# Kernel optimization log

Measured on AMD Instinct MI355X. Metric: run time of the kernel, lower is better.

Reference implementation:

```python
import jax, jax.numpy as jnp
import numpy as np

H = 64   # hidden size
V = 29   # vocab / feature size
SOS = 27 # start-token index set to 1 in the initial one-hot


def _cell(x, h, c, Wih, Whh, bih, bhh):
    # PyTorch LSTMCell gate order: i, f, g, o
    g = x @ Wih.T + h @ Whh.T + bih + bhh
    i, f, gg, o = jnp.split(g, 4, axis=-1)
    c = jax.nn.sigmoid(f) * c + jax.nn.sigmoid(i) * jnp.tanh(gg)
    h = jax.nn.sigmoid(o) * jnp.tanh(c)
    return h, c


def setup_inputs() -> dict:
    key = jax.random.key(0)
    ks = iter(jax.random.split(key, 32))
    T, B = 1024, 512
    def p(shape, scale=0.05):
        return jax.random.normal(next(ks), shape, dtype=jnp.float32) * scale
    inp = {"input_seq": jax.random.normal(next(ks), (T, B, V), dtype=jnp.float32)}
    inp.update(
        enc_Wih0=p((4 * H, V)), enc_Whh0=p((4 * H, H)), enc_bih0=p((4 * H,)), enc_bhh0=p((4 * H,)),
        enc_Wih1=p((4 * H, H)), enc_Whh1=p((4 * H, H)), enc_bih1=p((4 * H,)), enc_bhh1=p((4 * H,)),
        d1_Wih=p((4 * H, V)), d1_Whh=p((4 * H, H)), d1_bih=p((4 * H,)), d1_bhh=p((4 * H,)),
        d2_Wih=p((4 * H, H)), d2_Whh=p((4 * H, H)), d2_bih=p((4 * H,)), d2_bhh=p((4 * H,)),
        cls_W=p((V, H)), cls_b=p((V,)),
    )
    return inp


def reference(input_seq, enc_Wih0, enc_Whh0, enc_bih0, enc_bhh0,
              enc_Wih1, enc_Whh1, enc_bih1, enc_bhh1,
              d1_Wih, d1_Whh, d1_bih, d1_bhh,
              d2_Wih, d2_Whh, d2_bih, d2_bhh,
              cls_W, cls_b):
    T, B, _ = input_seq.shape
    dt = input_seq.dtype
    z = jnp.zeros((B, H), dt)

    def layer(x_seq, Wih, Whh, bih, bhh):
        def step(carry, x):
            h, c = _cell(x, carry[0], carry[1], Wih, Whh, bih, bhh)
            return (h, c), h
        (h, c), ys = jax.lax.scan(step, (z, z), x_seq)
        return ys, h, c

    # 2-layer encoder LSTM with zero initial state
    y1, _, _ = layer(input_seq, enc_Wih0, enc_Whh0, enc_bih0, enc_bhh0)
    _, h1, c1 = layer(y1, enc_Wih1, enc_Whh1, enc_bih1, enc_bhh1)  # top-layer final (h, c)

    let0 = jnp.zeros((B, V), dt).at[:, SOS].set(1.0)

    def dec_step(carry, _):
        h1, c1, h2, c2, let = carry
        h1, c1 = _cell(let, h1, c1, d1_Wih, d1_Whh, d1_bih, d1_bhh)
        h2, c2 = _cell(h1, h2, c2, d2_Wih, d2_Whh, d2_bih, d2_bhh)
        pred = h2 @ cls_W.T + cls_b  # [B, V]
        idx = jnp.argmax(pred, axis=-1)  # [B]
        # Faithful to original bug: sets column idx[b] to 1 for ALL rows, for each b
        let = jnp.zeros((B, V), pred.dtype).at[:, idx].set(1.0)
        return (h1, c1, h2, c2, let), pred

    _, outputs = jax.lax.scan(dec_step, (h1, c1, z, z, let0), None, length=T)
    return outputs  # [T, B, V]
```

## Files before the change

kernel.cpp:

```cpp
#include <hip/hip_runtime.h>
#include <math.h>

#define TSTEPS 1024
#define BATCH  512
#define HID    64
#define VOC    29
#define SOS    27
#define MASK29 0x1FFFFFFFu

#define ENC_BLOCKS 256
#define DEC_BLOCKS 256
#define NTHREADS   512

__device__ __forceinline__ float frcp(float x){ return __builtin_amdgcn_rcpf(x); }
__device__ __forceinline__ float sigmf(float x){ return frcp(1.0f + __expf(-x)); }
__device__ __forceinline__ float tanhfast(float x){ return 1.0f - 2.0f*frcp(1.0f + __expf(2.0f*x)); }

__global__ __attribute__((amdgpu_flat_work_group_size(NTHREADS,NTHREADS), amdgpu_waves_per_eu(2,2)))
void enc_kernel(const float* __restrict__ x,
                const float* __restrict__ Wih0, const float* __restrict__ Whh0,
                const float* __restrict__ bih0, const float* __restrict__ bhh0,
                const float* __restrict__ Wih1, const float* __restrict__ Whh1,
                const float* __restrict__ bih1, const float* __restrict__ bhh1,
                float* __restrict__ h1g, float* __restrict__ c1g)
{
  const int tid = threadIdx.x;
  const int b0  = blockIdx.x * 2;
  const bool g0 = tid < 256;
  const int  r  = g0 ? tid : (tid-256);

  __shared__ __align__(16) float xs[2][32];
  __shared__ __align__(16) float h0s[2][HID], h1s[2][HID];
  __shared__ __align__(16) float gA[2][256], gB[2][256];

  float wh[64], w2[64];
  if (g0){
    #pragma unroll
    for (int k=0;k<64;k++) wh[k] = Whh0[r*64+k];
    #pragma unroll
    for (int k=0;k<29;k++) w2[k] = Wih0[r*29+k];
    #pragma unroll
    for (int k=29;k<64;k++) w2[k] = 0.f;
  } else {
    #pragma unroll
    for (int k=0;k<64;k++){ wh[k] = Whh1[r*64+k]; w2[k] = Wih1[r*64+k]; }
  }
  const float bias = g0 ? (bih0[r]+bhh0[r]) : (bih1[r]+bhh1[r]);

  float creg = 0.f;
  if (tid < 128){ int u=tid>>6,k=tid&63; h0s[u][k]=0.f; h1s[u][k]=0.f; }

  const int pidx = tid - 448;
  const bool pf  = (pidx >= 0) && (pidx < 2*VOC);
  const int prow = pf ? (pidx/VOC) : 0;
  const int pcol = pf ? (pidx%VOC) : 0;
  if (pf) xs[prow][pcol] = x[(size_t)(b0+prow)*VOC + pcol];
  __syncthreads();

  for (int t=0;t<=TSTEPS;t++){
    float xv = 0.f;
    if (pf && t+1 < TSTEPS)
      xv = x[(size_t)(t+1)*BATCH*VOC + (size_t)(b0+prow)*VOC + pcol];

    if (g0){
      if (t < TSTEPS){
        #pragma unroll
        for (int u=0;u<2;u++){
          float a0=bias,a1=0.f,a2=0.f,a3=0.f;
          const float4* xv4 = (const float4*)xs[u];
          #pragma unroll
          for (int c=0;c<7;c++){
            float4 q=xv4[c];
            a0=fmaf(q.x,w2[4*c+0],a0); a1=fmaf(q.y,w2[4*c+1],a1);
            a2=fmaf(q.z,w2[4*c+2],a2); a3=fmaf(q.w,w2[4*c+3],a3);
          }
          a0=fmaf(xs[u][28],w2[28],a0);
          const float4* h4=(const float4*)h0s[u];
          #pragma unroll
          for (int c=0;c<16;c++){
            float4 q=h4[c];
            a0=fmaf(q.x,wh[4*c+0],a0); a1=fmaf(q.y,wh[4*c+1],a1);
            a2=fmaf(q.z,wh[4*c+2],a2); a3=fmaf(q.w,wh[4*c+3],a3);
          }
          gA[u][r]=(a0+a1)+(a2+a3);
        }
      }
    } else {
      if (t >= 1){
        #pragma unroll
        for (int u=0;u<2;u++){
          float a0=bias,a1=0.f,a2=0.f,a3=0.f;
          const float4* i4=(const float4*)h0s[u];
          const float4* h4=(const float4*)h1s[u];
          #pragma unroll
          for (int c=0;c<16;c++){
            float4 q=i4[c], w=h4[c];
            a0=fmaf(q.x,w2[4*c+0],a0); a1=fmaf(q.y,w2[4*c+1],a1);
            a2=fmaf(q.z,w2[4*c+2],a2); a3=fmaf(q.w,w2[4*c+3],a3);
            a0=fmaf(w.x,wh[4*c+0],a0); a1=fmaf(w.y,wh[4*c+1],a1);
            a2=fmaf(w.z,wh[4*c+2],a2); a3=fmaf(w.w,wh[4*c+3],a3);
          }
          gB[u][r]=(a0+a1)+(a2+a3);
        }
      }
    }
    __syncthreads();
    if (tid < 128){
      if (t < TSTEPS){
        int u=tid>>6,k=tid&63;
        float ig=gA[u][k],fg=gA[u][64+k],gg=gA[u][128+k],og=gA[u][192+k];
        float c=sigmf(fg)*creg + sigmf(ig)*tanhfast(gg);
        creg=c; h0s[u][k]=sigmf(og)*tanhfast(c);
      }
    } else if (tid < 384){
      if (t >= 1){
        int tt=tid-256,u=tt>>6,k=tt&63;
        float ig=gB[u][k],fg=gB[u][64+k],gg=gB[u][128+k],og=gB[u][192+k];
        float c=sigmf(fg)*creg + sigmf(ig)*tanhfast(gg);
        creg=c; h1s[u][k]=sigmf(og)*tanhfast(c);
      }
    }
    if (pf && t+1 < TSTEPS) xs[prow][pcol] = xv;
    __syncthreads();
  }

  if (tid >= 256 && tid < 384){
    int tt=tid-256,u=tt>>6,k=tt&63;
    h1g[(b0+u)*HID+k]=h1s[u][k];
    c1g[(b0+u)*HID+k]=creg;
  }
}

__global__ __attribute__((amdgpu_flat_work_group_size(NTHREADS,NTHREADS), amdgpu_waves_per_eu(2,2)))
void dec_kernel(const float* __restrict__ h1gp, const float* __restrict__ c1gp,
                const float* __restrict__ W1ih, const float* __restrict__ W1hh,
                const float* __restrict__ b1ih, const float* __restrict__ b1hh,
                const float* __restrict__ W2ih, const float* __restrict__ W2hh,
                const float* __restrict__ b2ih, const float* __restrict__ b2hh,
                const float* __restrict__ clsW, const float* __restrict__ clsb,
                float* __restrict__ out,
                unsigned long long* __restrict__ lvl1)
{
  const int tid  = threadIdx.x;
  const int r    = tid >> 1;
  const int p    = tid & 1;
  const int b0   = blockIdx.x * 2;
  const unsigned grp = blockIdx.x & 15;
  const unsigned idx = blockIdx.x >> 4;

  __shared__ __align__(16) float clsW_s[VOC][68];
  __shared__ __align__(16) float clsb_s[32];
  __shared__ __align__(16) float gl[2][256];
  __shared__ __align__(16) float h1s[2][HID], h2s[2][HID];
  __shared__ unsigned maskLDS;

  for (int i=tid;i<VOC*HID;i+=NTHREADS) clsW_s[i/HID][i%HID] = clsW[i];
  if (tid<VOC) clsb_s[tid]=clsb[tid];

  float w1h[32], w2i[32], w2h[32], wi1c[15];
  #pragma unroll
  for (int k=0;k<32;k++){
    w1h[k]=W1hh[r*HID+32*p+k];
    w2i[k]=W2ih[r*HID+32*p+k];
    w2h[k]=W2hh[r*HID+32*p+k];
  }
  const int cbase = p ? 15 : 0;
  const int cn    = p ? 14 : 15;
  #pragma unroll
  for (int j=0;j<15;j++) wi1c[j] = (j<cn) ? W1ih[r*VOC+cbase+j] : 0.f;
  const float biasg = p ? 0.f : (b1ih[r]+b1hh[r]);
  const float bias2 = p ? 0.f : (b2ih[r]+b2hh[r]);

  float c1reg=0.f, c2reg=0.f;
  if (tid<128){
    int u=tid>>6,k=tid&63;
    h1s[u][k]=h1gp[(b0+u)*HID+k];
    c1reg    =c1gp[(b0+u)*HID+k];
    h2s[u][k]=0.f;
  }
  __syncthreads();

  float hd1[2];
  #pragma unroll
  for (int u=0;u<2;u++){
    float a0=0.f,a1=0.f,a2=0.f,a3=0.f;
    const float4* h4=(const float4*)(h1s[u]+32*p);
    #pragma unroll
    for (int c=0;c<8;c++){
      float4 q=h4[c];
      a0=fmaf(q.x,w1h[4*c+0],a0); a1=fmaf(q.y,w1h[4*c+1],a1);
      a2=fmaf(q.z,w1h[4*c+2],a2); a3=fmaf(q.w,w1h[4*c+3],a3);
    }
    hd1[u]=(a0+a1)+(a2+a3);
  }

  unsigned mask = 1u<<SOS;

  for (int s=0;s<TSTEPS;s++){
    #pragma unroll
    for (int u=0;u<2;u++){
      float it = biasg;
      #pragma unroll
      for (int j=0;j<15;j++)
        it += ((mask>>(cbase+j))&1u) ? wi1c[j] : 0.f;
      float v = it + hd1[u];
      v += __shfl_xor(v,1);
      if (!p) gl[u][r] = v;
    }
    __syncthreads();
    if (tid<128){
      int u=tid>>6,k=tid&63;
      float ig=gl[u][k],fg=gl[u][64+k],gg=gl[u][128+k],og=gl[u][192+k];
      float c=sigmf(fg)*c1reg+sigmf(ig)*tanhfast(gg);
      c1reg=c; h1s[u][k]=sigmf(og)*tanhfast(c);
    }
    __syncthreads();
    #pragma unroll
    for (int u=0;u<2;u++){
      float a0=bias2,a1=0.f,a2=0.f,a3=0.f;
      const float4* i4=(const float4*)(h1s[u]+32*p);
      const float4* h4=(const float4*)(h2s[u]+32*p);
      #pragma unroll
      for (int c=0;c<8;c++){
        float4 q=i4[c], w=h4[c];
        a0=fmaf(q.x,w2i[4*c+0],a0); a1=fmaf(q.y,w2i[4*c+1],a1);
        a2=fmaf(q.z,w2i[4*c+2],a2); a3=fmaf(q.w,w2i[4*c+3],a3);
        a0=fmaf(w.x,w2h[4*c+0],a0); a1=fmaf(w.y,w2h[4*c+1],a1);
        a2=fmaf(w.z,w2h[4*c+2],a2); a3=fmaf(w.w,w2h[4*c+3],a3);
      }
      float v=(a0+a1)+(a2+a3);
      v += __shfl_xor(v,1);
      if (!p) gl[u][r]=v;
    }
    __syncthreads();
    if (tid<128){
      int u=tid>>6,k=tid&63;
      float ig=gl[u][k],fg=gl[u][64+k],gg=gl[u][128+k],og=gl[u][192+k];
      float c=sigmf(fg)*c2reg+sigmf(ig)*tanhfast(gg);
      c2reg=c; h2s[u][k]=sigmf(og)*tanhfast(c);
    }
    __syncthreads();
    if (tid<64){
      int row=tid>>5, v=tid&31;
      float pv = -INFINITY;
      if (v<VOC){
        float a0=clsb_s[v],a1=0.f,a2=0.f,a3=0.f;
        const float4* h4=(const float4*)h2s[row];
        #pragma unroll
        for (int c=0;c<16;c++){
          float4 q=h4[c];
          a0=fmaf(q.x,clsW_s[v][4*c+0],a0); a1=fmaf(q.y,clsW_s[v][4*c+1],a1);
          a2=fmaf(q.z,clsW_s[v][4*c+2],a2); a3=fmaf(q.w,clsW_s[v][4*c+3],a3);
        }
        pv=(a0+a1)+(a2+a3);
        out[((size_t)s*BATCH + (size_t)(b0+row))*VOC + v]=pv;
      }
      int ix=v;
      #pragma unroll
      for (int off=16; off>0; off>>=1){
        float ov=__shfl_xor(pv,off);
        int   oi=__shfl_xor(ix,off);
        if (ov>pv || (ov==pv && oi<ix)){ pv=ov; ix=oi; }
      }
      unsigned bit = 1u<<ix;
      unsigned mb  = bit | __shfl_xor(bit,32);
      if (tid==0 && s+1<TSTEPS)
        __hip_atomic_fetch_or(&lvl1[(size_t)grp*TSTEPS+s],
                              (unsigned long long)mb | (1ULL<<(32+idx)),
                              __ATOMIC_RELAXED, __HIP_MEMORY_SCOPE_AGENT);
    }
    if (s+1<TSTEPS){
      #pragma unroll
      for (int u=0;u<2;u++){
        float a0=0.f,a1=0.f,a2=0.f,a3=0.f;
        const float4* h4=(const float4*)(h1s[u]+32*p);
        #pragma unroll
        for (int c=0;c<8;c++){
          float4 q=h4[c];
          a0=fmaf(q.x,w1h[4*c+0],a0); a1=fmaf(q.y,w1h[4*c+1],a1);
          a2=fmaf(q.z,w1h[4*c+2],a2); a3=fmaf(q.w,w1h[4*c+3],a3);
        }
        hd1[u]=(a0+a1)+(a2+a3);
      }
      if (tid<64){
        while (true){
          unsigned long long u64 = 0;
          if (tid<16)
            u64 = __hip_atomic_load(&lvl1[(size_t)tid*TSTEPS+s],
                                    __ATOMIC_RELAXED, __HIP_MEMORY_SCOPE_AGENT);
          bool ok = (tid>=16) || ((unsigned)(u64>>32) == 0xFFFFu);
          if (__ballot(ok) == ~0ull){
            unsigned m = (tid<16) ? ((unsigned)u64 & MASK29) : 0u;
            m |= __shfl_xor(m,1); m |= __shfl_xor(m,2);
            m |= __shfl_xor(m,4); m |= __shfl_xor(m,8);
            if (tid==0) maskLDS = m;
            break;
          }
        }
      }
      __syncthreads();
      mask = maskLDS;
    }
  }
}

extern "C" void kernel_launch(void* const* d_in, const int* in_sizes, int n_in,
                              void* d_out, int out_size, void* d_ws, size_t ws_size,
                              hipStream_t stream)
{
  const float* x     = (const float*)d_in[0];
  const float* eWih0 = (const float*)d_in[1];
  const float* eWhh0 = (const float*)d_in[2];
  const float* ebih0 = (const float*)d_in[3];
  const float* ebhh0 = (const float*)d_in[4];
  const float* eWih1 = (const float*)d_in[5];
  const float* eWhh1 = (const float*)d_in[6];
  const float* ebih1 = (const float*)d_in[7];
  const float* ebhh1 = (const float*)d_in[8];
  const float* d1Wih = (const float*)d_in[9];
  const float* d1Whh = (const float*)d_in[10];
  const float* d1bih = (const float*)d_in[11];
  const float* d1bhh = (const float*)d_in[12];
  const float* d2Wih = (const float*)d_in[13];
  const float* d2Whh = (const float*)d_in[14];
  const float* d2bih = (const float*)d_in[15];
  const float* d2bhh = (const float*)d_in[16];
  const float* clsW  = (const float*)d_in[17];
  const float* clsb  = (const float*)d_in[18];
  float* out = (float*)d_out;

  float* h1g = (float*)d_ws;
  float* c1g = h1g + BATCH*HID;
  unsigned long long* lvl1 = (unsigned long long*)((char*)d_ws + (size_t)(2*BATCH*HID)*sizeof(float));

  hipMemsetAsync(lvl1, 0, 16*TSTEPS*sizeof(unsigned long long), stream);

  enc_kernel<<<ENC_BLOCKS, NTHREADS, 0, stream>>>(
      x, eWih0,eWhh0,ebih0,ebhh0, eWih1,eWhh1,ebih1,ebhh1, h1g,c1g);

  void* args[] = { (void*)&h1g, (void*)&c1g,
                   (void*)&d1Wih,(void*)&d1Whh,(void*)&d1bih,(void*)&d1bhh,
                   (void*)&d2Wih,(void*)&d2Whh,(void*)&d2bih,(void*)&d2bhh,
                   (void*)&clsW,(void*)&clsb,(void*)&out,(void*)&lvl1 };
  hipLaunchCooperativeKernel((void*)dec_kernel, dim3(DEC_BLOCKS), dim3(NTHREADS),
                             args, 0, stream);
}
```

Measured before the change: 5.822 ms.

## Speculate constant decoder mask over adaptive windows with verification and rollback

Replaces the per-step grid-wide mask exchange with speculative execution. Each block runs a window of decoder steps assuming the one-hot feedback mask stays unchanged, publishing each step's argmax bits. A single flag barrier at the end of the window then checks whether any step's combined mask differed. The window doubles, up to 16 steps, while speculation holds. On a mismatch the kernel restores checkpointed state and replays only the valid prefix. This trades one global sync per step for one per window, at the cost of wasted work and replay when the mask changes often.

```diff
diff --git a/kernel.cpp b/kernel.cpp
--- a/kernel.cpp
+++ b/kernel.cpp
@@ -6,11 +6,11 @@
 #define HID    64
 #define VOC    29
 #define SOS    27
-#define MASK29 0x1FFFFFFFu
 
 #define ENC_BLOCKS 256
 #define DEC_BLOCKS 256
 #define NTHREADS   512
+#define WMAX       16
 
 __device__ __forceinline__ float frcp(float x){ return __builtin_amdgcn_rcpf(x); }
 __device__ __forceinline__ float sigmf(float x){ return frcp(1.0f + __expf(-x)); }
@@ -139,20 +139,20 @@
                 const float* __restrict__ b2ih, const float* __restrict__ b2hh,
                 const float* __restrict__ clsW, const float* __restrict__ clsb,
                 float* __restrict__ out,
-                unsigned long long* __restrict__ lvl1)
+                unsigned* __restrict__ flags, unsigned* __restrict__ masks)
 {
   const int tid  = threadIdx.x;
   const int r    = tid >> 1;
   const int p    = tid & 1;
   const int b0   = blockIdx.x * 2;
-  const unsigned grp = blockIdx.x & 15;
-  const unsigned idx = blockIdx.x >> 4;
+  const int blk  = blockIdx.x;
 
   __shared__ __align__(16) float clsW_s[VOC][68];
   __shared__ __align__(16) float clsb_s[32];
   __shared__ __align__(16) float gl[2][256];
   __shared__ __align__(16) float h1s[2][HID], h2s[2][HID];
-  __shared__ unsigned maskLDS;
+  __shared__ __align__(16) float h1ck[2][HID], h2ck[2][HID];
+  __shared__ unsigned u_lds[WMAX];
 
   for (int i=tid;i<VOC*HID;i+=NTHREADS) clsW_s[i/HID][i%HID] = clsW[i];
   if (tid<VOC) clsb_s[tid]=clsb[tid];
@@ -194,82 +194,94 @@
     hd1[u]=(a0+a1)+(a2+a3);
   }
 
-  unsigned mask = 1u<<SOS;
-
-  for (int s=0;s<TSTEPS;s++){
-    #pragma unroll
-    for (int u=0;u<2;u++){
-      float it = biasg;
+  unsigned F = 1u<<SOS;
+  int f = 0;
+  unsigned rr = 0;
+  int Wcur = 4;
+
+  while (f < TSTEPS){
+    const int Wr = (TSTEPS - f < Wcur) ? (TSTEPS - f) : Wcur;
+
+    const float c1ck=c1reg, c2ck=c2reg, hd10=hd1[0], hd11=hd1[1];
+    if (tid<128){ int u=tid>>6,k=tid&63; h1ck[u][k]=h1s[u][k]; h2ck[u][k]=h2s[u][k]; }
+
+    float it0 = biasg;
+    #pragma unroll
+    for (int jj=0;jj<15;jj++) it0 += ((F>>(cbase+jj))&1u) ? wi1c[jj] : 0.f;
+
+    unsigned* __restrict__ mrow = masks + (rr&1u)*(WMAX*256);
+
+    for (int j=0;j<Wr;j++){
       #pragma unroll
-      for (int j=0;j<15;j++)
-        it += ((mask>>(cbase+j))&1u) ? wi1c[j] : 0.f;
-      float v = it + hd1[u];
-      v += __shfl_xor(v,1);
-      if (!p) gl[u][r] = v;
-    }
-    __syncthreads();
-    if (tid<128){
-      int u=tid>>6,k=tid&63;
-      float ig=gl[u][k],fg=gl[u][64+k],gg=gl[u][128+k],og=gl[u][192+k];
-      float c=sigmf(fg)*c1reg+sigmf(ig)*tanhfast(gg);
-      c1reg=c; h1s[u][k]=sigmf(og)*tanhfast(c);
-    }
-    __syncthreads();
-    #pragma unroll
-    for (int u=0;u<2;u++){
-      float a0=bias2,a1=0.f,a2=0.f,a3=0.f;
-      const float4* i4=(const float4*)(h1s[u]+32*p);
-      const float4* h4=(const float4*)(h2s[u]+32*p);
+      for (int u=0;u<2;u++){
+        float v = it0 + hd1[u];
+        v += __shfl_xor(v,1);
+        if (!p) gl[u][r] = v;
+      }
+      __syncthreads();
+      if (tid<128){
+        int u=tid>>6,k=tid&63;
+        float ig=gl[u][k],fg=gl[u][64+k],gg=gl[u][128+k],og=gl[u][192+k];
+        float c=sigmf(fg)*c1reg+sigmf(ig)*tanhfast(gg);
+        c1reg=c; h1s[u][k]=sigmf(og)*tanhfast(c);
+      }
+      __syncthreads();
       #pragma unroll
-      for (int c=0;c<8;c++){
-        float4 q=i4[c], w=h4[c];
-        a0=fmaf(q.x,w2i[4*c+0],a0); a1=fmaf(q.y,w2i[4*c+1],a1);
-        a2=fmaf(q.z,w2i[4*c+2],a2); a3=fmaf(q.w,w2i[4*c+3],a3);
-        a0=fmaf(w.x,w2h[4*c+0],a0); a1=fmaf(w.y,w2h[4*c+1],a1);
-        a2=fmaf(w.z,w2h[4*c+2],a2); a3=fmaf(w.w,w2h[4*c+3],a3);
-      }
-      float v=(a0+a1)+(a2+a3);
-      v += __shfl_xor(v,1);
-      if (!p) gl[u][r]=v;
-    }
-    __syncthreads();
-    if (tid<128){
-      int u=tid>>6,k=tid&63;
-      float ig=gl[u][k],fg=gl[u][64+k],gg=gl[u][128+k],og=gl[u][192+k];
-      float c=sigmf(fg)*c2reg+sigmf(ig)*tanhfast(gg);
-      c2reg=c; h2s[u][k]=sigmf(og)*tanhfast(c);
-    }
-    __syncthreads();
-    if (tid<64){
-      int row=tid>>5, v=tid&31;
-      float pv = -INFINITY;
-      if (v<VOC){
-        float a0=clsb_s[v],a1=0.f,a2=0.f,a3=0.f;
-        const float4* h4=(const float4*)h2s[row];
-        #pragma unroll
-        for (int c=0;c<16;c++){
-          float4 q=h4[c];
-          a0=fmaf(q.x,clsW_s[v][4*c+0],a0); a1=fmaf(q.y,clsW_s[v][4*c+1],a1);
-          a2=fmaf(q.z,clsW_s[v][4*c+2],a2); a3=fmaf(q.w,clsW_s[v][4*c+3],a3);
-        }
-        pv=(a0+a1)+(a2+a3);
-        out[((size_t)s*BATCH + (size_t)(b0+row))*VOC + v]=pv;
-      }
-      int ix=v;
-      #pragma unroll
-      for (int off=16; off>0; off>>=1){
-        float ov=__shfl_xor(pv,off);
-        int   oi=__shfl_xor(ix,off);
-        if (ov>pv || (ov==pv && oi<ix)){ pv=ov; ix=oi; }
-      }
-      unsigned bit = 1u<<ix;
-      unsigned mb  = bit | __shfl_xor(bit,32);
-      if (tid==0 && s+1<TSTEPS)
-        __hip_atomic_fetch_or(&lvl1[(size_t)grp*TSTEPS+s],
-                              (unsigned long long)mb | (1ULL<<(32+idx)),
-                              __ATOMIC_RELAXED, __HIP_MEMORY_SCOPE_AGENT);
-    }
-    if (s+1<TSTEPS){
+      for (int u=0;u<2;u++){
+        float a0=bias2,a1=0.f,a2=0.f,a3=0.f;
+        const float4* i4=(const float4*)(h1s[u]+32*p);
+        const float4* h4=(const float4*)(h2s[u]+32*p);
+        #pragma unroll
+        for (int c=0;c<8;c++){
+          float4 q=i4[c], w=h4[c];
+          a0=fmaf(q.x,w2i[4*c+0],a0); a1=fmaf(q.y,w2i[4*c+1],a1);
+          a2=fmaf(q.z,w2i[4*c+2],a2); a3=fmaf(q.w,w2i[4*c+3],a3);
+          a0=fmaf(w.x,w2h[4*c+0],a0); a1=fmaf(w.y,w2h[4*c+1],a1);
+          a2=fmaf(w.z,w2h[4*c+2],a2); a3=fmaf(w.w,w2h[4*c+3],a3);
+        }
+        float v=(a0+a1)+(a2+a3);
+        v += __shfl_xor(v,1);
+        if (!p) gl[u][r]=v;
+      }
+      __syncthreads();
+      if (tid<128){
+        int u=tid>>6,k=tid&63;
+        float ig=gl[u][k],fg=gl[u][64+k],gg=gl[u][128+k],og=gl[u][192+k];
+        float c=sigmf(fg)*c2reg+sigmf(ig)*tanhfast(gg);
+        c2reg=c; h2s[u][k]=sigmf(og)*tanhfast(c);
+      }
+      __syncthreads();
+      if (tid<64){
+        const int s = f + j;
+        int row=tid>>5, v=tid&31;
+        float pv = -INFINITY;
+        if (v<VOC){
+          float a0=clsb_s[v],a1=0.f,a2=0.f,a3=0.f;
+          const float4* h4=(const float4*)h2s[row];
+          #pragma unroll
+          for (int c=0;c<16;c++){
+            float4 q=h4[c];
+            a0=fmaf(q.x,clsW_s[v][4*c+0],a0); a1=fmaf(q.y,clsW_s[v][4*c+1],a1);
+            a2=fmaf(q.z,clsW_s[v][4*c+2],a2); a3=fmaf(q.w,clsW_s[v][4*c+3],a3);
+          }
+          pv=(a0+a1)+(a2+a3);
+          out[((size_t)s*BATCH + (size_t)(b0+row))*VOC + v]=pv;
+        }
+        int ix=v;
+        #pragma unroll
+        for (int off=16; off>0; off>>=1){
+          float ov=__shfl_xor(pv,off);
+          int   oi=__shfl_xor(ix,off);
+          if (ov>pv || (ov==pv && oi<ix)){ pv=ov; ix=oi; }
+        }
+        unsigned bit = 1u<<ix;
+        unsigned mb  = bit | __shfl_xor(bit,32);
+        if (tid==0){
+          __hip_atomic_store(&mrow[j*256+blk], mb, __ATOMIC_RELAXED, __HIP_MEMORY_SCOPE_AGENT);
+          if (j==Wr-1)
+            __hip_atomic_store(&flags[blk], rr+1u, __ATOMIC_RELEASE, __HIP_MEMORY_SCOPE_AGENT);
+        }
+      }
       #pragma unroll
       for (int u=0;u<2;u++){
         float a0=0.f,a1=0.f,a2=0.f,a3=0.f;
@@ -282,24 +294,103 @@
         }
         hd1[u]=(a0+a1)+(a2+a3);
       }
-      if (tid<64){
-        while (true){
-          unsigned long long u64 = 0;
-          if (tid<16)
-            u64 = __hip_atomic_load(&lvl1[(size_t)tid*TSTEPS+s],
-                                    __ATOMIC_RELAXED, __HIP_MEMORY_SCOPE_AGENT);
-          bool ok = (tid>=16) || ((unsigned)(u64>>32) == 0xFFFFu);
-          if (__ballot(ok) == ~0ull){
-            unsigned m = (tid<16) ? ((unsigned)u64 & MASK29) : 0u;
-            m |= __shfl_xor(m,1); m |= __shfl_xor(m,2);
-            m |= __shfl_xor(m,4); m |= __shfl_xor(m,8);
-            if (tid==0) maskLDS = m;
-            break;
-          }
-        }
-      }
-      __syncthreads();
-      mask = maskLDS;
+    }
+
+    if (tid<64){
+      const unsigned tgt = rr+1u;
+      for(;;){
+        unsigned a=__hip_atomic_load(&flags[tid    ],__ATOMIC_RELAXED,__HIP_MEMORY_SCOPE_AGENT);
+        unsigned b=__hip_atomic_load(&flags[tid+ 64],__ATOMIC_RELAXED,__HIP_MEMORY_SCOPE_AGENT);
+        unsigned c=__hip_atomic_load(&flags[tid+128],__ATOMIC_RELAXED,__HIP_MEMORY_SCOPE_AGENT);
+        unsigned d=__hip_atomic_load(&flags[tid+192],__ATOMIC_RELAXED,__HIP_MEMORY_SCOPE_AGENT);
+        bool ok = (a>=tgt)&&(b>=tgt)&&(c>=tgt)&&(d>=tgt);
+        if (__ballot(ok)==~0ull) break;
+      }
+      __threadfence();
+    }
+    __syncthreads();
+
+    {
+      const int j = tid>>5, sub = tid&31;
+      if (j < Wr){
+        unsigned* mp = mrow + j*256;
+        unsigned um=0;
+        #pragma unroll
+        for (int q=0;q<8;q++)
+          um |= __hip_atomic_load(&mp[q*32+sub],__ATOMIC_RELAXED,__HIP_MEMORY_SCOPE_AGENT);
+        um |= __shfl_xor(um,1); um |= __shfl_xor(um,2);
+        um |= __shfl_xor(um,4); um |= __shfl_xor(um,8); um |= __shfl_xor(um,16);
+        if (sub==0) u_lds[j]=um;
+      }
+    }
+    __syncthreads();
+
+    int jstar = Wr;
+    for (int jj=1;jj<Wr;jj++){ if (u_lds[jj-1]!=F){ jstar=jj; break; } }
+
+    if (jstar==Wr){
+      F = u_lds[Wr-1];
+      f += Wr; rr++;
+      Wcur = (2*Wcur>WMAX)?WMAX:2*Wcur;
+    } else {
+      c1reg=c1ck; c2reg=c2ck; hd1[0]=hd10; hd1[1]=hd11;
+      if (tid<128){ int u=tid>>6,k=tid&63; h1s[u][k]=h1ck[u][k]; h2s[u][k]=h2ck[u][k]; }
+      for (int j2=0;j2<jstar;j2++){
+        #pragma unroll
+        for (int u=0;u<2;u++){
+          float v = it0 + hd1[u];
+          v += __shfl_xor(v,1);
+          if (!p) gl[u][r] = v;
+        }
+        __syncthreads();
+        if (tid<128){
+          int u=tid>>6,k=tid&63;
+          float ig=gl[u][k],fg=gl[u][64+k],gg=gl[u][128+k],og=gl[u][192+k];
+          float c=sigmf(fg)*c1reg+sigmf(ig)*tanhfast(gg);
+          c1reg=c; h1s[u][k]=sigmf(og)*tanhfast(c);
+        }
+        __syncthreads();
+        #pragma unroll
+        for (int u=0;u<2;u++){
+          float a0=bias2,a1=0.f,a2=0.f,a3=0.f;
+          const float4* i4=(const float4*)(h1s[u]+32*p);
+          const float4* h4=(const float4*)(h2s[u]+32*p);
+          #pragma unroll
+          for (int c=0;c<8;c++){
+            float4 q=i4[c], w=h4[c];
+            a0=fmaf(q.x,w2i[4*c+0],a0); a1=fmaf(q.y,w2i[4*c+1],a1);
+            a2=fmaf(q.z,w2i[4*c+2],a2); a3=fmaf(q.w,w2i[4*c+3],a3);
+            a0=fmaf(w.x,w2h[4*c+0],a0); a1=fmaf(w.y,w2h[4*c+1],a1);
+            a2=fmaf(w.z,w2h[4*c+2],a2); a3=fmaf(w.w,w2h[4*c+3],a3);
+          }
+          float v=(a0+a1)+(a2+a3);
+          v += __shfl_xor(v,1);
+          if (!p) gl[u][r]=v;
+        }
+        __syncthreads();
+        if (tid<128){
+          int u=tid>>6,k=tid&63;
+          float ig=gl[u][k],fg=gl[u][64+k],gg=gl[u][128+k],og=gl[u][192+k];
+          float c=sigmf(fg)*c2reg+sigmf(ig)*tanhfast(gg);
+          c2reg=c; h2s[u][k]=sigmf(og)*tanhfast(c);
+        }
+        __syncthreads();
+        #pragma unroll
+        for (int u=0;u<2;u++){
+          float a0=0.f,a1=0.f,a2=0.f,a3=0.f;
+          const float4* h4=(const float4*)(h1s[u]+32*p);
+          #pragma unroll
+          for (int c=0;c<8;c++){
+            float4 q=h4[c];
+            a0=fmaf(q.x,w1h[4*c+0],a0); a1=fmaf(q.y,w1h[4*c+1],a1);
+            a2=fmaf(q.z,w1h[4*c+2],a2); a3=fmaf(q.w,w1h[4*c+3],a3);
+          }
+          hd1[u]=(a0+a1)+(a2+a3);
+        }
+      }
+      F = u_lds[jstar-1];
+      f += jstar; rr++;
+      Wcur = jstar;
     }
   }
 }
@@ -331,9 +422,10 @@
 
   float* h1g = (float*)d_ws;
   float* c1g = h1g + BATCH*HID;
-  unsigned long long* lvl1 = (unsigned long long*)((char*)d_ws + (size_t)(2*BATCH*HID)*sizeof(float));
-
-  hipMemsetAsync(lvl1, 0, 16*TSTEPS*sizeof(unsigned long long), stream);
+  unsigned* flags = (unsigned*)(c1g + BATCH*HID);
+  unsigned* masks = flags + 256;
+
+  hipMemsetAsync(flags, 0, 256*sizeof(unsigned), stream);
 
   enc_kernel<<<ENC_BLOCKS, NTHREADS, 0, stream>>>(
       x, eWih0,eWhh0,ebih0,ebhh0, eWih1,eWhh1,ebih1,ebhh1, h1g,c1g);
@@ -341,7 +433,8 @@
   void* args[] = { (void*)&h1g, (void*)&c1g,
                    (void*)&d1Wih,(void*)&d1Whh,(void*)&d1bih,(void*)&d1bhh,
                    (void*)&d2Wih,(void*)&d2Whh,(void*)&d2bih,(void*)&d2bhh,
-                   (void*)&clsW,(void*)&clsb,(void*)&out,(void*)&lvl1 };
+                   (void*)&clsW,(void*)&clsb,(void*)&out,
+                   (void*)&flags,(void*)&masks };
   hipLaunchCooperativeKernel((void*)dec_kernel, dim3(DEC_BLOCKS), dim3(NTHREADS),
                              args, 0, stream);
 }
```

Measured after the change: 4.847 ms. 16.8% less time.

## Speculate decoder steps with a constant letter mask and roll back on mismatch

Applied to the files above, without the earlier changes.

The decoder now runs a window of steps assuming the global argmax mask stays unchanged, writes each step's per-block mask with a round tag, and only does a grid-wide check after the window. If any step's global mask differs from the assumed one, state is restored from per-step checkpoints in shared memory and execution resumes from the first wrong step. The window size grows adaptively. Gate rows are also regrouped so each 8-lane group holds all four gates, which removes the shared-memory gate exchange and one barrier per cell. This trades the per-step grid synchronization for wasted recomputation whenever the argmax mask changes, and adds checkpoint stores and LDS usage.

```diff
diff --git a/kernel.cpp b/kernel.cpp
--- a/kernel.cpp
+++ b/kernel.cpp
@@ -11,6 +11,7 @@
 #define ENC_BLOCKS 256
 #define DEC_BLOCKS 256
 #define NTHREADS   512
+#define WMAX       16
 
 __device__ __forceinline__ float frcp(float x){ return __builtin_amdgcn_rcpf(x); }
 __device__ __forceinline__ float sigmf(float x){ return frcp(1.0f + __expf(-x)); }
@@ -139,20 +140,23 @@
                 const float* __restrict__ b2ih, const float* __restrict__ b2hh,
                 const float* __restrict__ clsW, const float* __restrict__ clsb,
                 float* __restrict__ out,
-                unsigned long long* __restrict__ lvl1)
+                unsigned long long* __restrict__ mseq)
 {
   const int tid  = threadIdx.x;
+  const int p    = tid & 1;
   const int r    = tid >> 1;
-  const int p    = tid & 1;
-  const int b0   = blockIdx.x * 2;
-  const unsigned grp = blockIdx.x & 15;
-  const unsigned idx = blockIdx.x >> 4;
+  const int q    = r & 3;
+  const int m    = tid >> 3;
+  const int g    = q*64 + m;
+  const int blk  = blockIdx.x;
+  const int b0   = blk * 2;
 
   __shared__ __align__(16) float clsW_s[VOC][68];
   __shared__ __align__(16) float clsb_s[32];
-  __shared__ __align__(16) float gl[2][256];
-  __shared__ __align__(16) float h1s[2][HID], h2s[2][HID];
-  __shared__ unsigned maskLDS;
+  __shared__ __align__(16) float h1s[2][2][HID], h2s[2][2][HID];
+  __shared__ __align__(16) float h1ck[WMAX][2][HID], c1ck[WMAX][2][HID];
+  __shared__ __align__(16) float h2ck[WMAX][2][HID], c2ck[WMAX][2][HID];
+  __shared__ unsigned u_lds[WMAX];
 
   for (int i=tid;i<VOC*HID;i+=NTHREADS) clsW_s[i/HID][i%HID] = clsW[i];
   if (tid<VOC) clsb_s[tid]=clsb[tid];
@@ -160,147 +164,171 @@
   float w1h[32], w2i[32], w2h[32], wi1c[15];
   #pragma unroll
   for (int k=0;k<32;k++){
-    w1h[k]=W1hh[r*HID+32*p+k];
-    w2i[k]=W2ih[r*HID+32*p+k];
-    w2h[k]=W2hh[r*HID+32*p+k];
+    w1h[k]=W1hh[g*HID+32*p+k];
+    w2i[k]=W2ih[g*HID+32*p+k];
+    w2h[k]=W2hh[g*HID+32*p+k];
   }
   const int cbase = p ? 15 : 0;
   const int cn    = p ? 14 : 15;
   #pragma unroll
-  for (int j=0;j<15;j++) wi1c[j] = (j<cn) ? W1ih[r*VOC+cbase+j] : 0.f;
-  const float biasg = p ? 0.f : (b1ih[r]+b1hh[r]);
-  const float bias2 = p ? 0.f : (b2ih[r]+b2hh[r]);
-
-  float c1reg=0.f, c2reg=0.f;
+  for (int j=0;j<15;j++) wi1c[j] = (j<cn) ? W1ih[g*VOC+cbase+j] : 0.f;
+  const float biasg = p ? 0.f : (b1ih[g]+b1hh[g]);
+  const float bias2 = p ? 0.f : (b2ih[g]+b2hh[g]);
+
+  float c1r[2], c2r[2];
+  c1r[0]=c1gp[(b0+0)*HID+m]; c1r[1]=c1gp[(b0+1)*HID+m];
+  c2r[0]=0.f; c2r[1]=0.f;
   if (tid<128){
     int u=tid>>6,k=tid&63;
-    h1s[u][k]=h1gp[(b0+u)*HID+k];
-    c1reg    =c1gp[(b0+u)*HID+k];
-    h2s[u][k]=0.f;
+    h1s[0][u][k]=h1gp[(b0+u)*HID+k];
+    h2s[0][u][k]=0.f;
   }
   __syncthreads();
 
-  float hd1[2];
-  #pragma unroll
-  for (int u=0;u<2;u++){
-    float a0=0.f,a1=0.f,a2=0.f,a3=0.f;
-    const float4* h4=(const float4*)(h1s[u]+32*p);
-    #pragma unroll
-    for (int c=0;c<8;c++){
-      float4 q=h4[c];
-      a0=fmaf(q.x,w1h[4*c+0],a0); a1=fmaf(q.y,w1h[4*c+1],a1);
-      a2=fmaf(q.z,w1h[4*c+2],a2); a3=fmaf(q.w,w1h[4*c+3],a3);
-    }
-    hd1[u]=(a0+a1)+(a2+a3);
-  }
-
-  unsigned mask = 1u<<SOS;
-
-  for (int s=0;s<TSTEPS;s++){
-    #pragma unroll
-    for (int u=0;u<2;u++){
-      float it = biasg;
-      #pragma unroll
-      for (int j=0;j<15;j++)
-        it += ((mask>>(cbase+j))&1u) ? wi1c[j] : 0.f;
-      float v = it + hd1[u];
-      v += __shfl_xor(v,1);
-      if (!p) gl[u][r] = v;
-    }
-    __syncthreads();
-    if (tid<128){
-      int u=tid>>6,k=tid&63;
-      float ig=gl[u][k],fg=gl[u][64+k],gg=gl[u][128+k],og=gl[u][192+k];
-      float c=sigmf(fg)*c1reg+sigmf(ig)*tanhfast(gg);
-      c1reg=c; h1s[u][k]=sigmf(og)*tanhfast(c);
-    }
-    __syncthreads();
-    #pragma unroll
-    for (int u=0;u<2;u++){
-      float a0=bias2,a1=0.f,a2=0.f,a3=0.f;
-      const float4* i4=(const float4*)(h1s[u]+32*p);
-      const float4* h4=(const float4*)(h2s[u]+32*p);
-      #pragma unroll
-      for (int c=0;c<8;c++){
-        float4 q=i4[c], w=h4[c];
-        a0=fmaf(q.x,w2i[4*c+0],a0); a1=fmaf(q.y,w2i[4*c+1],a1);
-        a2=fmaf(q.z,w2i[4*c+2],a2); a3=fmaf(q.w,w2i[4*c+3],a3);
-        a0=fmaf(w.x,w2h[4*c+0],a0); a1=fmaf(w.y,w2h[4*c+1],a1);
-        a2=fmaf(w.z,w2h[4*c+2],a2); a3=fmaf(w.w,w2h[4*c+3],a3);
-      }
-      float v=(a0+a1)+(a2+a3);
-      v += __shfl_xor(v,1);
-      if (!p) gl[u][r]=v;
-    }
-    __syncthreads();
-    if (tid<128){
-      int u=tid>>6,k=tid&63;
-      float ig=gl[u][k],fg=gl[u][64+k],gg=gl[u][128+k],og=gl[u][192+k];
-      float c=sigmf(fg)*c2reg+sigmf(ig)*tanhfast(gg);
-      c2reg=c; h2s[u][k]=sigmf(og)*tanhfast(c);
-    }
-    __syncthreads();
-    if (tid<64){
-      int row=tid>>5, v=tid&31;
-      float pv = -INFINITY;
-      if (v<VOC){
-        float a0=clsb_s[v],a1=0.f,a2=0.f,a3=0.f;
-        const float4* h4=(const float4*)h2s[row];
-        #pragma unroll
-        for (int c=0;c<16;c++){
-          float4 q=h4[c];
-          a0=fmaf(q.x,clsW_s[v][4*c+0],a0); a1=fmaf(q.y,clsW_s[v][4*c+1],a1);
-          a2=fmaf(q.z,clsW_s[v][4*c+2],a2); a3=fmaf(q.w,clsW_s[v][4*c+3],a3);
-        }
-        pv=(a0+a1)+(a2+a3);
-        out[((size_t)s*BATCH + (size_t)(b0+row))*VOC + v]=pv;
-      }
-      int ix=v;
-      #pragma unroll
-      for (int off=16; off>0; off>>=1){
-        float ov=__shfl_xor(pv,off);
-        int   oi=__shfl_xor(ix,off);
-        if (ov>pv || (ov==pv && oi<ix)){ pv=ov; ix=oi; }
-      }
-      unsigned bit = 1u<<ix;
-      unsigned mb  = bit | __shfl_xor(bit,32);
-      if (tid==0 && s+1<TSTEPS)
-        __hip_atomic_fetch_or(&lvl1[(size_t)grp*TSTEPS+s],
-                              (unsigned long long)mb | (1ULL<<(32+idx)),
-                              __ATOMIC_RELAXED, __HIP_MEMORY_SCOPE_AGENT);
-    }
-    if (s+1<TSTEPS){
+  unsigned F = 1u<<SOS;
+  int f = 0;
+  unsigned rr = 0;
+  int Wcur = 4, streak = 0;
+  int pb = 0;
+
+  while (f < TSTEPS){
+    const int Wr = (TSTEPS - f < Wcur) ? (TSTEPS - f) : Wcur;
+    const unsigned tag = rr + 1u;
+    unsigned long long* __restrict__ mrow = mseq + (size_t)(rr&1u)*(WMAX*256);
+
+    if (tid < Wr) u_lds[tid] = 0u;
+
+    float it0 = biasg;
+    #pragma unroll
+    for (int jj=0;jj<15;jj++) it0 += ((F>>(cbase+jj))&1u) ? wi1c[jj] : 0.f;
+
+    for (int j=0;j<Wr;j++){
+      float h1n[2];
       #pragma unroll
       for (int u=0;u<2;u++){
-        float a0=0.f,a1=0.f,a2=0.f,a3=0.f;
-        const float4* h4=(const float4*)(h1s[u]+32*p);
+        float a0=it0,a1=0.f,a2=0.f,a3=0.f;
+        const float4* h4=(const float4*)(&h1s[pb][u][32*p]);
         #pragma unroll
         for (int c=0;c<8;c++){
-          float4 q=h4[c];
-          a0=fmaf(q.x,w1h[4*c+0],a0); a1=fmaf(q.y,w1h[4*c+1],a1);
-          a2=fmaf(q.z,w1h[4*c+2],a2); a3=fmaf(q.w,w1h[4*c+3],a3);
-        }
-        hd1[u]=(a0+a1)+(a2+a3);
-      }
+          float4 qv=h4[c];
+          a0=fmaf(qv.x,w1h[4*c+0],a0); a1=fmaf(qv.y,w1h[4*c+1],a1);
+          a2=fmaf(qv.z,w1h[4*c+2],a2); a3=fmaf(qv.w,w1h[4*c+3],a3);
+        }
+        float v=(a0+a1)+(a2+a3);
+        v += __shfl_xor(v,1);
+        float x2=__shfl_xor(v,2), x4=__shfl_xor(v,4), x6=__shfl_xor(v,6);
+        float ig = q==0?v : q==1?x2 : q==2?x4 : x6;
+        float fg = q==1?v : q==0?x2 : q==3?x4 : x6;
+        float gg = q==2?v : q==3?x2 : q==0?x4 : x6;
+        float og = q==3?v : q==2?x2 : q==1?x4 : x6;
+        float c = sigmf(fg)*c1r[u] + sigmf(ig)*tanhfast(gg);
+        c1r[u]=c; h1n[u]=sigmf(og)*tanhfast(c);
+      }
+      if ((tid&7)==0){
+        h1s[pb^1][0][m]=h1n[0]; h1s[pb^1][1][m]=h1n[1];
+        h1ck[j][0][m]=h1n[0];   h1ck[j][1][m]=h1n[1];
+        c1ck[j][0][m]=c1r[0];   c1ck[j][1][m]=c1r[1];
+      }
+      __syncthreads();
+
+      float h2n[2];
+      #pragma unroll
+      for (int u=0;u<2;u++){
+        float a0=bias2,a1=0.f,a2=0.f,a3=0.f;
+        const float4* i4=(const float4*)(&h1s[pb^1][u][32*p]);
+        const float4* h4=(const float4*)(&h2s[pb][u][32*p]);
+        #pragma unroll
+        for (int c=0;c<8;c++){
+          float4 qv=i4[c], wv=h4[c];
+          a0=fmaf(qv.x,w2i[4*c+0],a0); a1=fmaf(qv.y,w2i[4*c+1],a1);
+          a2=fmaf(qv.z,w2i[4*c+2],a2); a3=fmaf(qv.w,w2i[4*c+3],a3);
+          a0=fmaf(wv.x,w2h[4*c+0],a0); a1=fmaf(wv.y,w2h[4*c+1],a1);
+          a2=fmaf(wv.z,w2h[4*c+2],a2); a3=fmaf(wv.w,w2h[4*c+3],a3);
+        }
+        float v=(a0+a1)+(a2+a3);
+        v += __shfl_xor(v,1);
+        float x2=__shfl_xor(v,2), x4=__shfl_xor(v,4), x6=__shfl_xor(v,6);
+        float ig = q==0?v : q==1?x2 : q==2?x4 : x6;
+        float fg = q==1?v : q==0?x2 : q==3?x4 : x6;
+        float gg = q==2?v : q==3?x2 : q==0?x4 : x6;
+        float og = q==3?v : q==2?x2 : q==1?x4 : x6;
+        float c = sigmf(fg)*c2r[u] + sigmf(ig)*tanhfast(gg);
+        c2r[u]=c; h2n[u]=sigmf(og)*tanhfast(c);
+      }
+      if ((tid&7)==0){
+        h2s[pb^1][0][m]=h2n[0]; h2s[pb^1][1][m]=h2n[1];
+        h2ck[j][0][m]=h2n[0];   h2ck[j][1][m]=h2n[1];
+        c2ck[j][0][m]=c2r[0];   c2ck[j][1][m]=c2r[1];
+      }
+      __syncthreads();
+
       if (tid<64){
-        while (true){
-          unsigned long long u64 = 0;
-          if (tid<16)
-            u64 = __hip_atomic_load(&lvl1[(size_t)tid*TSTEPS+s],
-                                    __ATOMIC_RELAXED, __HIP_MEMORY_SCOPE_AGENT);
-          bool ok = (tid>=16) || ((unsigned)(u64>>32) == 0xFFFFu);
-          if (__ballot(ok) == ~0ull){
-            unsigned m = (tid<16) ? ((unsigned)u64 & MASK29) : 0u;
-            m |= __shfl_xor(m,1); m |= __shfl_xor(m,2);
-            m |= __shfl_xor(m,4); m |= __shfl_xor(m,8);
-            if (tid==0) maskLDS = m;
-            break;
+        const int s = f + j;
+        int row=tid>>5, v=tid&31;
+        float pv = -INFINITY;
+        if (v<VOC){
+          float a0=clsb_s[v],a1=0.f,a2=0.f,a3=0.f;
+          const float4* h4=(const float4*)h2s[pb^1][row];
+          #pragma unroll
+          for (int c=0;c<16;c++){
+            float4 qv=h4[c];
+            a0=fmaf(qv.x,clsW_s[v][4*c+0],a0); a1=fmaf(qv.y,clsW_s[v][4*c+1],a1);
+            a2=fmaf(qv.z,clsW_s[v][4*c+2],a2); a3=fmaf(qv.w,clsW_s[v][4*c+3],a3);
           }
-        }
-      }
-      __syncthreads();
-      mask = maskLDS;
-    }
+          pv=(a0+a1)+(a2+a3);
+          out[((size_t)s*BATCH + (size_t)(b0+row))*VOC + v]=pv;
+        }
+        int ix=v;
+        #pragma unroll
+        for (int off=16; off>0; off>>=1){
+          float ov=__shfl_xor(pv,off);
+          int   oi=__shfl_xor(ix,off);
+          if (ov>pv || (ov==pv && oi<ix)){ pv=ov; ix=oi; }
+        }
+        unsigned bit = 1u<<ix;
+        unsigned mb  = bit | __shfl_xor(bit,32);
+        if (tid==0)
+          __hip_atomic_store(&mrow[j*256+blk],
+                             ((unsigned long long)tag<<32) | (unsigned long long)mb,
+                             __ATOMIC_RELAXED, __HIP_MEMORY_SCOPE_AGENT);
+      }
+      pb ^= 1;
+    }
+
+    for (int w=tid; w<Wr*256; w+=NTHREADS){
+      const int jj = w>>8, bb = w&255;
+      unsigned long long vv;
+      do {
+        vv = __hip_atomic_load(&mrow[jj*256+bb], __ATOMIC_RELAXED, __HIP_MEMORY_SCOPE_AGENT);
+      } while ((unsigned)(vv>>32) != tag);
+      unsigned um = (unsigned)vv & MASK29;
+      um |= __shfl_xor(um,1);  um |= __shfl_xor(um,2);  um |= __shfl_xor(um,4);
+      um |= __shfl_xor(um,8);  um |= __shfl_xor(um,16); um |= __shfl_xor(um,32);
+      if ((tid&63)==0) atomicOr(&u_lds[jj], um);
+    }
+    __syncthreads();
+
+    int jstar = Wr;
+    for (int jj=1;jj<Wr;jj++){ if (u_lds[jj-1]!=F){ jstar=jj; break; } }
+
+    if (jstar==Wr){
+      F = u_lds[Wr-1]; f += Wr; rr++;
+      streak++;
+      if (streak>=2 && Wcur<WMAX) Wcur*=2;
+    } else {
+      const int jm = jstar-1;
+      c1r[0]=c1ck[jm][0][m]; c1r[1]=c1ck[jm][1][m];
+      c2r[0]=c2ck[jm][0][m]; c2r[1]=c2ck[jm][1][m];
+      if (tid<128){
+        int u=tid>>6,k=tid&63;
+        h1s[0][u][k]=h1ck[jm][u][k];
+        h2s[0][u][k]=h2ck[jm][u][k];
+      }
+      pb = 0;
+      F = u_lds[jm]; f += jstar; rr++;
+      streak = 0; Wcur = jstar;
+    }
+    __syncthreads();
   }
 }
 
@@ -331,9 +359,10 @@
 
   float* h1g = (float*)d_ws;
   float* c1g = h1g + BATCH*HID;
-  unsigned long long* lvl1 = (unsigned long long*)((char*)d_ws + (size_t)(2*BATCH*HID)*sizeof(float));
-
-  hipMemsetAsync(lvl1, 0, 16*TSTEPS*sizeof(unsigned long long), stream);
+  unsigned long long* mseq =
+      (unsigned long long*)((char*)d_ws + (size_t)(2*BATCH*HID)*sizeof(float));
+
+  hipMemsetAsync(mseq, 0, (size_t)2*WMAX*256*sizeof(unsigned long long), stream);
 
   enc_kernel<<<ENC_BLOCKS, NTHREADS, 0, stream>>>(
       x, eWih0,eWhh0,ebih0,ebhh0, eWih1,eWhh1,ebih1,ebhh1, h1g,c1g);
@@ -341,7 +370,8 @@
   void* args[] = { (void*)&h1g, (void*)&c1g,
                    (void*)&d1Wih,(void*)&d1Whh,(void*)&d1bih,(void*)&d1bhh,
                    (void*)&d2Wih,(void*)&d2Whh,(void*)&d2bih,(void*)&d2bhh,
-                   (void*)&clsW,(void*)&clsb,(void*)&out,(void*)&lvl1 };
+                   (void*)&clsW,(void*)&clsb,(void*)&out,
+                   (void*)&mseq };
   hipLaunchCooperativeKernel((void*)dec_kernel, dim3(DEC_BLOCKS), dim3(NTHREADS),
                              args, 0, stream);
 }
```

New measurement: 4.874 ms. -16.3%, faster.
